# Performance work log

Hardware: AMD Instinct MI355X
Metric: run time of the kernel (lower is better)

Reference implementation:

```python
import jax, jax.numpy as jnp
import numpy as np

INPUT_DIM = 66
OUTPUT_COUNT = 8192
NUM_PAIRS = 65536

def setup_inputs() -> dict:
    key = jax.random.key(0)
    k1, k2, k3, k4 = jax.random.split(key, 4)
    x = jax.random.normal(k1, (NUM_PAIRS, INPUT_DIM), dtype=jnp.float32)
    query = jax.random.normal(k2, (OUTPUT_COUNT, INPUT_DIM), dtype=jnp.float32)
    # nn.Linear(input_dim, input_dim): weight [out,in], bias [out]
    bound = 1.0 / np.sqrt(INPUT_DIM)
    Wk = jax.random.uniform(k3, (INPUT_DIM, INPUT_DIM), minval=-bound, maxval=bound, dtype=jnp.float32)
    bk = jax.random.uniform(k4, (INPUT_DIM,), minval=-bound, maxval=bound, dtype=jnp.float32)
    return {"x": x, "query": query, "Wk": Wk, "bk": bk}

def reference(x, query, Wk, bk):
    # K = Linear(x): x @ Wk^T + bk  -> [num_pairs, d]
    K = x @ Wk.T + bk
    # scores: [output_count, num_pairs]
    scores = jnp.einsum("qd,nd->qn", query, K)
    attn = jax.nn.softmax(scores, axis=1)
    # selected: [output_count, d] — note values are raw x, not K
    selected = attn @ x
    return selected
```

## Files before the change

### kernel.cpp

```cpp
#include <hip/hip_runtime.h>
#include <cstdint>


typedef __bf16    bf16x4 __attribute__((ext_vector_type(4)));
typedef __bf16    bf16x8 __attribute__((ext_vector_type(8)));
typedef _Float16  f16x4  __attribute__((ext_vector_type(4)));
typedef _Float16  f16x8  __attribute__((ext_vector_type(8)));
typedef float     f32x16 __attribute__((ext_vector_type(16)));

extern "C" __device__ float __ocml_native_exp2_f32(float);

#define NUM_PAIRS   65536
#define NUM_Q       8192
#define DIM         66
#define KPITCH      84
#define QPITCH      80
#define XROWS       96
#define XPITCH      36
#define XTILE       (XROWS*XPITCH)
#define PARTP       68

#define LDS_XT 5376
#define STG     12288
#define KSTRIDE 5376
#define XSTRIDE 6912

__device__ __forceinline__ bf16x8 frag8(const __bf16* p) {
    bf16x4 lo = *(const bf16x4*)p;
    bf16x4 hi = *(const bf16x4*)(p + 4);
    return __builtin_shufflevector(lo, hi, 0, 1, 2, 3, 4, 5, 6, 7);
}
__device__ __forceinline__ f16x8 frag8h(const _Float16* p) {
    f16x4 lo = *(const f16x4*)p;
    f16x4 hi = *(const f16x4*)(p + 4);
    return __builtin_shufflevector(lo, hi, 0, 1, 2, 3, 4, 5, 6, 7);
}
__device__ __forceinline__ f32x16 mfma_bf16(bf16x8 a, bf16x8 b, f32x16 c) {
    return __builtin_amdgcn_mfma_f32_32x32x16_bf16(a, b, c, 0, 0, 0);
}
__device__ __forceinline__ f32x16 mfma_f16(f16x8 a, f16x8 b, f32x16 c) {
    return __builtin_amdgcn_mfma_f32_32x32x16_f16(a, b, c, 0, 0, 0);
}

__device__ __forceinline__ void plswap(unsigned &a, unsigned &b) {
    asm("v_permlane32_swap_b32 %0, %1" : "+v"(a), "+v"(b));
}
__device__ __forceinline__ unsigned packbf(float a, float b) {
    union { __bf16 h[2]; unsigned u; } t;
    t.h[0] = (__bf16)a; t.h[1] = (__bf16)b;
    return t.u;
}

union U4 { unsigned u[4]; bf16x8 v; };

__device__ __forceinline__ void makefrags(const f32x16 &s, U4 *f) {
    float P[16];
    #pragma unroll
    for (int r = 0; r < 16; ++r) P[r] = __ocml_native_exp2_f32(s[r]);
    unsigned E0 = packbf(P[0],  P[1]),  E1 = packbf(P[2],  P[3]);
    unsigned F0 = packbf(P[4],  P[5]),  F1 = packbf(P[6],  P[7]);
    plswap(E0, F0); plswap(E1, F1);
    f[0].u[0] = E0; f[0].u[1] = E1; f[0].u[2] = F0; f[0].u[3] = F1;
    unsigned G0 = packbf(P[8],  P[9]),  G1 = packbf(P[10], P[11]);
    unsigned H0 = packbf(P[12], P[13]), H1 = packbf(P[14], P[15]);
    plswap(G0, H0); plswap(G1, H1);
    f[1].u[0] = G0; f[1].u[1] = G1; f[1].u[2] = H0; f[1].u[3] = H1;
}

__device__ __forceinline__ void stage_tile(char* dst, const char* gK, const char* gX,
                                           int wave, int lane) {
    #pragma unroll
    for (int j = 0; j < 3; ++j) {
        int c = wave + 4 * j;
        int off = c * 1024 + lane * 16;
        const char* src = (off < KSTRIDE) ? (gK + off) : (gX + (off - KSTRIDE));
        __builtin_amdgcn_global_load_lds(
            (const __attribute__((address_space(1))) void*)(uintptr_t)src,
            (__attribute__((address_space(3))) void*)(unsigned int)(uintptr_t)(dst + c * 1024),
            16, 0, 0);
    }
}

__device__ __forceinline__ void compute_tile(const char* sm, const f16x8 (&aQ)[5],
                                             f32x16 (&o)[3], int l31, int h) {
    const _Float16* Kt = (const _Float16*)sm;
    const __bf16*   Xt = (const __bf16*)(sm + LDS_XT);
    f16x8 bK[5];
    #pragma unroll
    for (int kk = 0; kk < 5; ++kk)
        bK[kk] = frag8h(&Kt[l31 * KPITCH + kk * 16 + h * 8]);
    f32x16 s = {};
    #pragma unroll
    for (int kk = 0; kk < 5; ++kk) s = mfma_f16(bK[kk], aQ[kk], s);
    U4 f[2];
    makefrags(s, f);
    #pragma unroll
    for (int par = 0; par < 2; ++par) {
        const int kc = par * 16 + h * 8;
        #pragma unroll
        for (int dt = 0; dt < 3; ++dt) {
            bf16x8 bX = frag8(&Xt[(dt * 32 + l31) * XPITCH + kc]);
            o[dt] = mfma_bf16(f[par].v, bX, o[dt]);
        }
    }
}

#define PA_ROWS 128
#define PAP 104
__global__ __launch_bounds__(256) void prep_kernel(
    const float* __restrict__ x, const float* __restrict__ query,
    const float* __restrict__ Wk, const float* __restrict__ bk,
    unsigned short* __restrict__ Kh_u, unsigned short* __restrict__ Xb_u,
    unsigned short* __restrict__ Qh_u) {
    const int tid = threadIdx.x;
    if (blockIdx.x >= 512) {
        _Float16* Qh = (_Float16*)Qh_u;
        int base = (blockIdx.x - 512) * 1280;
        #pragma unroll
        for (int k = 0; k < 5; ++k) {
            int idx = base + k * 256 + tid;
            int q = idx / QPITCH, c = idx % QPITCH;
            float v = (c < DIM) ? query[(long)q * DIM + c] * 1.4426950408889634f : 0.f;
            Qh[idx] = (_Float16)v;
        }
        return;
    }
    _Float16* Kh = (_Float16*)Kh_u;
    __bf16*   Xb = (__bf16*)Xb_u;
    __shared__ _Float16 sxh[PA_ROWS * PAP];
    __shared__ _Float16 sW[96 * PAP];
    const long n0 = (long)blockIdx.x * PA_ROWS;

    for (int i = tid; i < PA_ROWS * 96; i += 256) {
        int r = i / 96, c = i % 96;
        sxh[r * PAP + c] = (_Float16)((c < DIM) ? x[(n0 + r) * DIM + c] : 0.f);
    }
    for (int i = tid; i < 96 * 96; i += 256) {
        int cc = i / 96, d = i % 96;
        sW[cc * PAP + d] = (_Float16)((cc < DIM && d < DIM) ? Wk[cc * DIM + d] : 0.f);
    }
    __syncthreads();

    const int lane = tid & 63, w = tid >> 6;
    const int l31 = lane & 31, h = lane >> 5;

    #pragma unroll
    for (int nt = 0; nt < 3; ++nt) {
        f32x16 acc = {};
        #pragma unroll
        for (int kk = 0; kk < 6; ++kk) {
            f16x8 a = *(const f16x8*)&sxh[(w * 32 + l31) * PAP + kk * 16 + h * 8];
            f16x8 b = *(const f16x8*)&sW[(nt * 32 + l31) * PAP + kk * 16 + h * 8];
            acc = mfma_f16(a, b, acc);
        }
        int c = nt * 32 + l31;
        float bkv = (c < DIM) ? bk[c] : 0.f;
        if (c < KPITCH) {
            #pragma unroll
            for (int r = 0; r < 16; ++r) {
                int row = (r & 3) + 8 * (r >> 2) + 4 * h;
                Kh[(n0 + w * 32 + row) * KPITCH + c] = (_Float16)(acc[r] + bkv);
            }
        }
    }

    for (int ii = tid; ii < 4 * XTILE; ii += 256) {
        int b = ii / XTILE, i = ii % XTILE;
        int dd = i / XPITCH, j = i % XPITCH;
        float v = 0.f;
        if (j < 32) {
            if (dd < DIM) v = (float)sxh[(b * 32 + j) * PAP + dd];
            else if (dd == DIM) v = 1.f;
        }
        Xb[((long)blockIdx.x * 4 + b) * XTILE + i] = (__bf16)v;
    }
}

__global__ __launch_bounds__(256, 4) void flash_kernel(
    const unsigned short* __restrict__ Qh_u, const unsigned short* __restrict__ Kh_u,
    const unsigned short* __restrict__ Xb_u, float* __restrict__ Part, int NS) {
    __shared__ __attribute__((aligned(16))) char smA[STG];
    __shared__ __attribute__((aligned(16))) char smB[STG];
    const _Float16* Qh = (const _Float16*)Qh_u;

    const int tid = threadIdx.x;
    const int lane = tid & 63, wave = tid >> 6;
    const int l31 = lane & 31, h = lane >> 5;
    const int qb = blockIdx.x / NS, ns = blockIdx.x % NS;
    const int ppc = NUM_PAIRS / NS;
    const int iters = ppc >> 5;
    const int qbase = qb * 128 + wave * 32;

    const long pbase = (long)ns * ppc;
    const char* gK0 = (const char*)Kh_u + pbase * (KPITCH * 2);
    const char* gX0 = (const char*)Xb_u + (pbase >> 5) * (XTILE * 2);

    f16x8 aQ[5];
    #pragma unroll
    for (int kk = 0; kk < 5; ++kk)
        aQ[kk] = *(const f16x8*)&Qh[(long)(qbase + l31) * QPITCH + kk * 16 + h * 8];

    f32x16 o[3] = {};

    stage_tile(smA, gK0, gX0, wave, lane);
    for (int it = 0; it < iters; it += 2) {
        __syncthreads();
        if (it + 1 < iters)
            stage_tile(smB, gK0 + (long)(it + 1) * KSTRIDE,
                            gX0 + (long)(it + 1) * XSTRIDE, wave, lane);
        compute_tile(smA, aQ, o, l31, h);
        __syncthreads();
        if (it + 2 < iters)
            stage_tile(smA, gK0 + (long)(it + 2) * KSTRIDE,
                            gX0 + (long)(it + 2) * XSTRIDE, wave, lane);
        compute_tile(smB, aQ, o, l31, h);
    }

    float* dst = Part + (long)ns * NUM_Q * PARTP;
    #pragma unroll
    for (int dt = 0; dt < 3; ++dt)
        #pragma unroll
        for (int r = 0; r < 16; ++r) {
            int row = (r & 3) + 8 * (r >> 2) + 4 * h;
            int q = qbase + row;
            int d = dt * 32 + l31;
            if (d < DIM + 1) dst[(long)q * PARTP + d] = o[dt][r];
        }
}

__global__ __launch_bounds__(256) void combine_kernel(
    const float* __restrict__ Part, float* __restrict__ out, int NS) {
    int q = blockIdx.x * 2 + (threadIdx.x >> 7);
    int d = threadIdx.x & 127;
    if (d >= DIM) return;
    float num = 0.f, den = 0.f;
    #pragma unroll 4
    for (int s = 0; s < NS; ++s) {
        const float* p = Part + ((long)s * NUM_Q + q) * PARTP;
        num += p[d];
        den += p[DIM];
    }
    out[(long)q * DIM + d] = num / den;
}

extern "C" void kernel_launch(void* const* d_in, const int* in_sizes, int n_in,
                              void* d_out, int out_size, void* d_ws, size_t ws_size,
                              hipStream_t stream) {
    const float* x     = (const float*)d_in[0];
    const float* query = (const float*)d_in[1];
    const float* Wk    = (const float*)d_in[2];
    const float* bk    = (const float*)d_in[3];
    float* out = (float*)d_out;
    char* ws = (char*)d_ws;

    unsigned short* Qh = (unsigned short*)(ws + 0);
    unsigned short* Kh = (unsigned short*)(ws + 1310720);
    unsigned short* Xb = (unsigned short*)(ws + 12320768);
    float* Part        = (float*)(ws + 26476544);

    int NS = 16;
    while (NS > 1 &&
           26476544ULL + (unsigned long long)NS * NUM_Q * PARTP * 4ULL > (unsigned long long)ws_size)
        NS >>= 1;

    prep_kernel<<<1024, 256, 0, stream>>>(x, query, Wk, bk, Kh, Xb, Qh);
    flash_kernel<<<(NUM_Q / 128) * NS, 256, 0, stream>>>(Qh, Kh, Xb, Part, NS);
    combine_kernel<<<NUM_Q / 2, 256, 0, stream>>>(Part, out, NS);
}
```

Baseline: 305.2 us.

## Pre-swizzle K/X into MFMA fragment layout and load directly to registers

The prep kernel now writes K and X in a fragment-ordered layout, so each lane can load its MFMA operands with contiguous 16-byte global loads. This lets the flash kernel skip LDS staging and most barriers, and register double-buffer the K fragments instead. Each wave now handles 64 queries (two Q tiles), so every loaded K/X fragment is reused twice. The partial-sum layout is also changed to per-query-contiguous so the combine reads are coalesced. The cost is higher register pressure (occupancy hint drops from 4 to 2) and exposed global-load latency for X, which is not prefetched.

Result: faster. 280.1 us (-8.2%).

```diff
diff --git a/kernel.cpp b/kernel.cpp
--- a/kernel.cpp
+++ b/kernel.cpp
@@ -13,35 +13,18 @@
 #define NUM_PAIRS   65536
 #define NUM_Q       8192
 #define DIM         66
-#define KPITCH      84
 #define QPITCH      80
-#define XROWS       96
-#define XPITCH      36
-#define XTILE       (XROWS*XPITCH)
+#define KFT         2560
+#define XFT         3072
 #define PARTP       68
-
-#define LDS_XT 5376
-#define STG     12288
-#define KSTRIDE 5376
-#define XSTRIDE 6912
-
-__device__ __forceinline__ bf16x8 frag8(const __bf16* p) {
-    bf16x4 lo = *(const bf16x4*)p;
-    bf16x4 hi = *(const bf16x4*)(p + 4);
-    return __builtin_shufflevector(lo, hi, 0, 1, 2, 3, 4, 5, 6, 7);
-}
-__device__ __forceinline__ f16x8 frag8h(const _Float16* p) {
-    f16x4 lo = *(const f16x4*)p;
-    f16x4 hi = *(const f16x4*)(p + 4);
-    return __builtin_shufflevector(lo, hi, 0, 1, 2, 3, 4, 5, 6, 7);
-}
+#define NTILES      (NUM_PAIRS/32)
+
 __device__ __forceinline__ f32x16 mfma_bf16(bf16x8 a, bf16x8 b, f32x16 c) {
     return __builtin_amdgcn_mfma_f32_32x32x16_bf16(a, b, c, 0, 0, 0);
 }
 __device__ __forceinline__ f32x16 mfma_f16(f16x8 a, f16x8 b, f32x16 c) {
     return __builtin_amdgcn_mfma_f32_32x32x16_f16(a, b, c, 0, 0, 0);
 }
-
 __device__ __forceinline__ void plswap(unsigned &a, unsigned &b) {
     asm("v_permlane32_swap_b32 %0, %1" : "+v"(a), "+v"(b));
 }
@@ -50,7 +33,6 @@
     t.h[0] = (__bf16)a; t.h[1] = (__bf16)b;
     return t.u;
 }
-
 union U4 { unsigned u[4]; bf16x8 v; };
 
 __device__ __forceinline__ void makefrags(const f32x16 &s, U4 *f) {
@@ -67,50 +49,35 @@
     f[1].u[0] = G0; f[1].u[1] = G1; f[1].u[2] = H0; f[1].u[3] = H1;
 }
 
-__device__ __forceinline__ void stage_tile(char* dst, const char* gK, const char* gX,
-                                           int wave, int lane) {
-    #pragma unroll
-    for (int j = 0; j < 3; ++j) {
-        int c = wave + 4 * j;
-        int off = c * 1024 + lane * 16;
-        const char* src = (off < KSTRIDE) ? (gK + off) : (gX + (off - KSTRIDE));
-        __builtin_amdgcn_global_load_lds(
-            (const __attribute__((address_space(1))) void*)(uintptr_t)src,
-            (__attribute__((address_space(3))) void*)(unsigned int)(uintptr_t)(dst + c * 1024),
-            16, 0, 0);
-    }
-}
-
-__device__ __forceinline__ void compute_tile(const char* sm, const f16x8 (&aQ)[5],
-                                             f32x16 (&o)[3], int l31, int h) {
-    const _Float16* Kt = (const _Float16*)sm;
-    const __bf16*   Xt = (const __bf16*)(sm + LDS_XT);
-    f16x8 bK[5];
-    #pragma unroll
-    for (int kk = 0; kk < 5; ++kk)
-        bK[kk] = frag8h(&Kt[l31 * KPITCH + kk * 16 + h * 8]);
-    f32x16 s = {};
-    #pragma unroll
-    for (int kk = 0; kk < 5; ++kk) s = mfma_f16(bK[kk], aQ[kk], s);
-    U4 f[2];
-    makefrags(s, f);
-    #pragma unroll
-    for (int par = 0; par < 2; ++par) {
-        const int kc = par * 16 + h * 8;
+__device__ __forceinline__ void compute_tile(const f16x8 (&kc)[5], const __bf16* __restrict__ xp,
+                                             const f16x8 (&aQ)[2][5], f32x16 (&o)[2][3]) {
+    bf16x8 xa[6];
+    #pragma unroll
+    for (int c = 0; c < 6; ++c) xa[c] = *(const bf16x8*)(xp + c * 512);
+    f32x16 s0 = {}, s1 = {};
+    #pragma unroll
+    for (int kk = 0; kk < 5; ++kk) {
+        s0 = mfma_f16(kc[kk], aQ[0][kk], s0);
+        s1 = mfma_f16(kc[kk], aQ[1][kk], s1);
+    }
+    U4 f0[2], f1[2];
+    makefrags(s0, f0);
+    makefrags(s1, f1);
+    #pragma unroll
+    for (int par = 0; par < 2; ++par)
         #pragma unroll
         for (int dt = 0; dt < 3; ++dt) {
-            bf16x8 bX = frag8(&Xt[(dt * 32 + l31) * XPITCH + kc]);
-            o[dt] = mfma_bf16(f[par].v, bX, o[dt]);
-        }
-    }
-}
-
-#define PA_ROWS 128
+            o[0][dt] = mfma_bf16(f0[par].v, xa[par * 3 + dt], o[0][dt]);
+            o[1][dt] = mfma_bf16(f1[par].v, xa[par * 3 + dt], o[1][dt]);
+        }
+}
+
 #define PAP 104
+#define SKP 88
 __global__ __launch_bounds__(256) void prep_kernel(
     const float* __restrict__ x, const float* __restrict__ query,
     const float* __restrict__ Wk, const float* __restrict__ bk,
-    unsigned short* __restrict__ Kh_u, unsigned short* __restrict__ Xb_u,
+    unsigned short* __restrict__ Kf_u, unsigned short* __restrict__ Xf_u,
     unsigned short* __restrict__ Qh_u) {
     const int tid = threadIdx.x;
     if (blockIdx.x >= 512) {
@@ -125,13 +92,14 @@
         }
         return;
     }
-    _Float16* Kh = (_Float16*)Kh_u;
-    __bf16*   Xb = (__bf16*)Xb_u;
-    __shared__ _Float16 sxh[PA_ROWS * PAP];
+    _Float16* Kf = (_Float16*)Kf_u;
+    __bf16*   Xf = (__bf16*)Xf_u;
+    __shared__ _Float16 sxh[128 * PAP];
     __shared__ _Float16 sW[96 * PAP];
-    const long n0 = (long)blockIdx.x * PA_ROWS;
-
-    for (int i = tid; i < PA_ROWS * 96; i += 256) {
+    __shared__ _Float16 sK[128 * SKP];
+    const long n0 = (long)blockIdx.x * 128;
+
+    for (int i = tid; i < 128 * 96; i += 256) {
         int r = i / 96, c = i % 96;
         sxh[r * PAP + c] = (_Float16)((c < DIM) ? x[(n0 + r) * DIM + c] : 0.f);
     }
@@ -155,77 +123,103 @@
         }
         int c = nt * 32 + l31;
         float bkv = (c < DIM) ? bk[c] : 0.f;
-        if (c < KPITCH) {
+        if (c < SKP) {
             #pragma unroll
             for (int r = 0; r < 16; ++r) {
                 int row = (r & 3) + 8 * (r >> 2) + 4 * h;
-                Kh[(n0 + w * 32 + row) * KPITCH + c] = (_Float16)(acc[r] + bkv);
+                sK[(w * 32 + row) * SKP + c] = (_Float16)(acc[r] + bkv);
             }
         }
     }
-
-    for (int ii = tid; ii < 4 * XTILE; ii += 256) {
-        int b = ii / XTILE, i = ii % XTILE;
-        int dd = i / XPITCH, j = i % XPITCH;
-        float v = 0.f;
-        if (j < 32) {
-            if (dd < DIM) v = (float)sxh[(b * 32 + j) * PAP + dd];
-            else if (dd == DIM) v = 1.f;
-        }
-        Xb[((long)blockIdx.x * 4 + b) * XTILE + i] = (__bf16)v;
-    }
-}
-
-__global__ __launch_bounds__(256, 4) void flash_kernel(
-    const unsigned short* __restrict__ Qh_u, const unsigned short* __restrict__ Kh_u,
-    const unsigned short* __restrict__ Xb_u, float* __restrict__ Part, int NS) {
-    __shared__ __attribute__((aligned(16))) char smA[STG];
-    __shared__ __attribute__((aligned(16))) char smB[STG];
+    __syncthreads();
+
+    for (int i = 0; i < 5; ++i) {
+        int slot = i * 256 + tid;
+        int tt = slot / 320, rem = slot % 320;
+        int kk = rem / 64, l = rem % 64;
+        const _Float16* src = &sK[(32 * tt + (l & 31)) * SKP + kk * 16 + (l >> 5) * 8];
+        f16x4 lo = *(const f16x4*)src;
+        f16x4 hi = *(const f16x4*)(src + 4);
+        f16x8 v = __builtin_shufflevector(lo, hi, 0, 1, 2, 3, 4, 5, 6, 7);
+        *(f16x8*)&Kf[((long)blockIdx.x * 4 + tt) * KFT + kk * 512 + l * 8] = v;
+    }
+    for (int i = 0; i < 6; ++i) {
+        int slot = i * 256 + tid;
+        int tt = slot / 384, rem = slot % 384;
+        int c = rem / 64, l = rem % 64;
+        int dt = c % 3, par = c / 3;
+        int d = 32 * dt + (l & 31);
+        int p0 = 32 * tt + 16 * par + 8 * (l >> 5);
+        bf16x8 v;
+        #pragma unroll
+        for (int j = 0; j < 8; ++j) {
+            float vv = 0.f;
+            if (d < DIM) vv = (float)sxh[(p0 + j) * PAP + d];
+            else if (d == DIM) vv = 1.f;
+            v[j] = (__bf16)vv;
+        }
+        *(bf16x8*)&Xf[((long)blockIdx.x * 4 + tt) * XFT + c * 512 + l * 8] = v;
+    }
+}
+
+__global__ __launch_bounds__(256, 2) void flash_kernel(
+    const unsigned short* __restrict__ Qh_u, const unsigned short* __restrict__ Kf_u,
+    const unsigned short* __restrict__ Xf_u, float* __restrict__ Part, int NS) {
     const _Float16* Qh = (const _Float16*)Qh_u;
+    const _Float16* Kf = (const _Float16*)Kf_u;
+    const __bf16*   Xf = (const __bf16*)Xf_u;
 
     const int tid = threadIdx.x;
     const int lane = tid & 63, wave = tid >> 6;
     const int l31 = lane & 31, h = lane >> 5;
     const int qb = blockIdx.x / NS, ns = blockIdx.x % NS;
-    const int ppc = NUM_PAIRS / NS;
-    const int iters = ppc >> 5;
-    const int qbase = qb * 128 + wave * 32;
-
-    const long pbase = (long)ns * ppc;
-    const char* gK0 = (const char*)Kh_u + pbase * (KPITCH * 2);
-    const char* gX0 = (const char*)Xb_u + (pbase >> 5) * (XTILE * 2);
-
-    f16x8 aQ[5];
-    #pragma unroll
-    for (int kk = 0; kk < 5; ++kk)
-        aQ[kk] = *(const f16x8*)&Qh[(long)(qbase + l31) * QPITCH + kk * 16 + h * 8];
-
-    f32x16 o[3] = {};
-
-    stage_tile(smA, gK0, gX0, wave, lane);
-    for (int it = 0; it < iters; it += 2) {
-        __syncthreads();
-        if (it + 1 < iters)
-            stage_tile(smB, gK0 + (long)(it + 1) * KSTRIDE,
-                            gX0 + (long)(it + 1) * XSTRIDE, wave, lane);
-        compute_tile(smA, aQ, o, l31, h);
-        __syncthreads();
-        if (it + 2 < iters)
-            stage_tile(smA, gK0 + (long)(it + 2) * KSTRIDE,
-                            gX0 + (long)(it + 2) * XSTRIDE, wave, lane);
-        compute_tile(smB, aQ, o, l31, h);
-    }
-
-    float* dst = Part + (long)ns * NUM_Q * PARTP;
-    #pragma unroll
-    for (int dt = 0; dt < 3; ++dt)
-        #pragma unroll
-        for (int r = 0; r < 16; ++r) {
-            int row = (r & 3) + 8 * (r >> 2) + 4 * h;
-            int q = qbase + row;
-            int d = dt * 32 + l31;
-            if (d < DIM + 1) dst[(long)q * PARTP + d] = o[dt][r];
-        }
+    const int tiles = NTILES / NS;
+    const int qbase = qb * 256 + wave * 64;
+
+    const _Float16* kf = Kf + (long)(ns * tiles) * KFT + lane * 8;
+    const __bf16*   xf = Xf + (long)(ns * tiles) * XFT + lane * 8;
+
+    f16x8 aQ[2][5];
+    #pragma unroll
+    for (int qt = 0; qt < 2; ++qt)
+        #pragma unroll
+        for (int kk = 0; kk < 5; ++kk)
+            aQ[qt][kk] = *(const f16x8*)&Qh[(long)(qbase + qt * 32 + l31) * QPITCH + kk * 16 + h * 8];
+
+    f32x16 o[2][3] = {};
+
+    f16x8 kA[5], kB[5];
+    #pragma unroll
+    for (int kk = 0; kk < 5; ++kk) kA[kk] = *(const f16x8*)(kf + kk * 512);
+
+    for (int t = 0; t < tiles; t += 2) {
+        if ((t & 31) == 0) asm volatile("s_barrier");
+        {
+            const _Float16* kp = kf + (long)(t + 1) * KFT;
+            #pragma unroll
+            for (int kk = 0; kk < 5; ++kk) kB[kk] = *(const f16x8*)(kp + kk * 512);
+        }
+        compute_tile(kA, xf + (long)t * XFT, aQ, o);
+        if (t + 2 < tiles) {
+            const _Float16* kp = kf + (long)(t + 2) * KFT;
+            #pragma unroll
+            for (int kk = 0; kk < 5; ++kk) kA[kk] = *(const f16x8*)(kp + kk * 512);
+        }
+        compute_tile(kB, xf + (long)(t + 1) * XFT, aQ, o);
+    }
+
+    #pragma unroll
+    for (int qt = 0; qt < 2; ++qt)
+        #pragma unroll
+        for (int dt = 0; dt < 3; ++dt)
+            #pragma unroll
+            for (int r = 0; r < 16; ++r) {
+                int row = (r & 3) + 8 * (r >> 2) + 4 * h;
+                int q = qbase + qt * 32 + row;
+                int d = dt * 32 + l31;
+                if (d < DIM + 1)
+                    Part[((long)q * NS + ns) * PARTP + d] = o[qt][dt][r];
+            }
 }
 
 __global__ __launch_bounds__(256) void combine_kernel(
@@ -233,12 +227,12 @@
     int q = blockIdx.x * 2 + (threadIdx.x >> 7);
     int d = threadIdx.x & 127;
     if (d >= DIM) return;
+    const float* base = Part + (long)q * NS * PARTP;
     float num = 0.f, den = 0.f;
     #pragma unroll 4
     for (int s = 0; s < NS; ++s) {
-        const float* p = Part + ((long)s * NUM_Q + q) * PARTP;
-        num += p[d];
-        den += p[DIM];
+        num += base[s * PARTP + d];
+        den += base[s * PARTP + DIM];
     }
     out[(long)q * DIM + d] = num / den;
 }
@@ -254,16 +248,16 @@
     char* ws = (char*)d_ws;
 
     unsigned short* Qh = (unsigned short*)(ws + 0);
-    unsigned short* Kh = (unsigned short*)(ws + 1310720);
-    unsigned short* Xb = (unsigned short*)(ws + 12320768);
-    float* Part        = (float*)(ws + 26476544);
+    unsigned short* Kf = (unsigned short*)(ws + 1310720);
+    unsigned short* Xf = (unsigned short*)(ws + 11796480);
+    float* Part        = (float*)(ws + 24379392);
 
     int NS = 16;
     while (NS > 1 &&
-           26476544ULL + (unsigned long long)NS * NUM_Q * PARTP * 4ULL > (unsigned long long)ws_size)
+           24379392ULL + (unsigned long long)NS * NUM_Q * PARTP * 4ULL > (unsigned long long)ws_size)
         NS >>= 1;
 
-    prep_kernel<<<1024, 256, 0, stream>>>(x, query, Wk, bk, Kh, Xb, Qh);
-    flash_kernel<<<(NUM_Q / 128) * NS, 256, 0, stream>>>(Qh, Kh, Xb, Part, NS);
+    prep_kernel<<<1024, 256, 0, stream>>>(x, query, Wk, bk, Kf, Xf, Qh);
+    flash_kernel<<<(NUM_Q / 256) * NS, 256, 0, stream>>>(Qh, Kf, Xf, Part, NS);
     combine_kernel<<<NUM_Q / 2, 256, 0, stream>>>(Part, out, NS);
 }
```
